# Kernel optimization log

Hardware: AMD Instinct MI355X
Metric: run time of the kernel (lower is better)

The kernel has to match this reference:

```python
import jax, jax.numpy as jnp
import numpy as np

N_X, DIS, IN, OUT = 40000, 10000, 128, 64
N = N_X + DIS
E = 800000
BN_EPS = 1e-5


def setup_inputs() -> dict:
    key = jax.random.key(0)
    ks = jax.random.split(key, 20)

    def glorot(k, shape):
        fan_in, fan_out = shape[-2], shape[-1]
        a = np.sqrt(6.0 / (fan_in + fan_out)).astype(np.float32)
        return jax.random.uniform(k, shape, jnp.float32, -a, a)

    return {
        "x": jax.random.normal(ks[0], (N_X, IN), jnp.float32),
        "emb": jax.random.uniform(ks[1], (DIS, IN), jnp.float32),
        "conv1_w": glorot(ks[2], (3, IN, 2 * OUT)),
        "conv1_root": glorot(ks[3], (IN, 2 * OUT)),
        "conv1_bias": jnp.zeros((2 * OUT,), jnp.float32),
        "conv2_w": glorot(ks[4], (3, 2 * OUT, 4 * OUT)),
        "conv2_root": glorot(ks[5], (2 * OUT, 4 * OUT)),
        "conv2_bias": jnp.zeros((4 * OUT,), jnp.float32),
        "convinf_w": glorot(ks[6], (3, 4 * OUT, 4 * OUT)),
        "convinf_root": glorot(ks[7], (4 * OUT, 4 * OUT)),
        "convinf_bias": jnp.zeros((4 * OUT,), jnp.float32),
        "conv3_w": glorot(ks[8], (3, 4 * OUT, OUT)),
        "conv3_root": glorot(ks[9], (4 * OUT, OUT)),
        "conv3_bias": jnp.zeros((OUT,), jnp.float32),
        "norm1_g": jnp.ones((2 * OUT,), jnp.float32),
        "norm1_b": jnp.zeros((2 * OUT,), jnp.float32),
        "norm2_g": jnp.ones((4 * OUT,), jnp.float32),
        "norm2_b": jnp.zeros((4 * OUT,), jnp.float32),
        "edge_index": jax.random.randint(ks[10], (2, E), 0, N),
        "edge_types": jax.random.randint(ks[11], (E,), 0, 3),
    }


def reference(x, emb, conv1_w, conv1_root, conv1_bias, conv2_w, conv2_root,
              conv2_bias, convinf_w, convinf_root, convinf_bias, conv3_w,
              conv3_root, conv3_bias, norm1_g, norm1_b, norm2_g, norm2_b,
              edge_index, edge_types):
    dst, src = edge_index[0], edge_index[1]  # adj_t row = target, col = source
    n = x.shape[0] + emb.shape[0]

    # gcn_norm without self-loops: deg over rows, w_e = d^-1/2[dst] * d^-1/2[src]
    deg = jax.ops.segment_sum(jnp.ones(dst.shape[0], jnp.float32), dst, num_segments=n)
    dis = jnp.where(deg > 0, jax.lax.rsqrt(jnp.maximum(deg, 1.0)), 0.0)
    ew = dis[dst] * dis[src]  # [E]

    def wrgcn(h, W, root, bias):
        out = h @ root + bias
        h_src = h[src]  # [E, d] gather (dominant memory traffic)
        for r in range(3):
            w_r = jnp.where(edge_types == r, ew, 0.0)
            agg = jax.ops.segment_sum(w_r[:, None] * h_src, dst, num_segments=n)
            out = out + agg @ W[r]
        return out

    def bn(h, g, b):
        m = h.mean(axis=0)
        v = jnp.var(h, axis=0)  # biased, matches torch BN training normalization
        return (h - m) * jax.lax.rsqrt(v + BN_EPS) * g + b

    h0 = jnp.concatenate([x, emb], axis=0)  # [N, IN]
    x1 = bn(wrgcn(h0, conv1_w, conv1_root, conv1_bias), norm1_g, norm1_b)
    x2 = bn(wrgcn(jax.nn.relu(x1), conv2_w, conv2_root, conv2_bias), norm2_g, norm2_b)
    for _ in range(5):
        x2 = bn(wrgcn(jax.nn.relu(x2), convinf_w, convinf_root, convinf_bias), norm2_g, norm2_b)
    return wrgcn(jax.nn.relu(x2), conv3_w, conv3_root, conv3_bias)
```

## Files before the change

kernel.cpp:

```cpp
#include <hip/hip_runtime.h>

#define N_X  40000
#define NN   50000
#define NE   800000
#define MPAD 50048

using short8  = __attribute__((ext_vector_type(8))) short;
using floatx4 = __attribute__((ext_vector_type(4))) float;

typedef const __attribute__((address_space(1))) void gv_t;
typedef __attribute__((address_space(3))) void lv_t;

__device__ __forceinline__ unsigned short f2bf(float f) {
  unsigned u = __float_as_uint(f);
  u += 0x7FFF + ((u >> 16) & 1);
  return (unsigned short)(u >> 16);
}
__device__ __forceinline__ float bf2f(unsigned v) {
  return __uint_as_float(v << 16);
}

__global__ void k_deg(const int* __restrict__ dst, int* __restrict__ deg) {
  int e = blockIdx.x * blockDim.x + threadIdx.x;
  if (e < NE) atomicAdd(&deg[dst[e]], 1);
}

__global__ void k_dis(const int* __restrict__ deg, float* __restrict__ dis) {
  int i = blockIdx.x * blockDim.x + threadIdx.x;
  if (i < NN) dis[i] = deg[i] > 0 ? rsqrtf((float)deg[i]) : 0.f;
}

#define SCAN_B 1024
#define SCAN_NB 49
__global__ void k_scan1(const int* __restrict__ deg, int* __restrict__ rowp,
                        int* __restrict__ bsum) {
  __shared__ int buf[SCAN_B];
  int b = blockIdx.x;
  int i = b * SCAN_B + threadIdx.x;
  int v = (i < NN) ? deg[i] : 0;
  buf[threadIdx.x] = v;
  __syncthreads();
  for (int off = 1; off < SCAN_B; off <<= 1) {
    int t = (threadIdx.x >= off) ? buf[threadIdx.x - off] : 0;
    __syncthreads();
    buf[threadIdx.x] += t;
    __syncthreads();
  }
  if (i < NN) rowp[i] = buf[threadIdx.x] - v;
  if (threadIdx.x == SCAN_B - 1) bsum[b] = buf[SCAN_B - 1];
}

__global__ void k_scan2(int* __restrict__ bsum) {
  if (threadIdx.x == 0) {
    int acc = 0;
    for (int i = 0; i < SCAN_NB; ++i) { int t = bsum[i]; bsum[i] = acc; acc += t; }
  }
}

__global__ void k_scan3(int* __restrict__ rowp, const int* __restrict__ bsum) {
  int i = blockIdx.x * blockDim.x + threadIdx.x;
  if (i < NN) rowp[i] += bsum[i >> 10];
  if (i == 0) rowp[NN] = NE;
}

__global__ void k_build(const int* __restrict__ dst, const int* __restrict__ src,
                        const int* __restrict__ typ, const float* __restrict__ dis,
                        const int* __restrict__ rowp, int* __restrict__ cur,
                        unsigned* __restrict__ est, float* __restrict__ ewt) {
  int e = blockIdx.x * blockDim.x + threadIdx.x;
  if (e >= NE) return;
  int d = dst[e], s = src[e];
  int p = rowp[d] + atomicAdd(&cur[d], 1);
  est[p] = (unsigned)s | ((unsigned)typ[e] << 28);
  ewt[p] = dis[d] * dis[s];
}

__global__ void k_prep0(const float* __restrict__ x, const float* __restrict__ emb,
                        unsigned short* __restrict__ Xh, unsigned short* __restrict__ Xl,
                        int xs) {
  int idx = blockIdx.x * blockDim.x + threadIdx.x;
  if (idx >= NN * 32) return;
  int r = idx >> 5, c4 = (idx & 31) * 4;
  const float* srcp = (r < N_X) ? (x + (size_t)r * 128 + c4)
                                : (emb + (size_t)(r - N_X) * 128 + c4);
  float4 hv = *(const float4*)srcp;
  float vv[4] = {hv.x, hv.y, hv.z, hv.w};
  unsigned hw[2], lw[2];
#pragma unroll
  for (int q = 0; q < 2; ++q) {
    unsigned short h0 = f2bf(vv[2 * q]), h1 = f2bf(vv[2 * q + 1]);
    unsigned short l0 = f2bf(vv[2 * q] - bf2f(h0)), l1 = f2bf(vv[2 * q + 1] - bf2f(h1));
    hw[q] = (unsigned)h0 | ((unsigned)h1 << 16);
    lw[q] = (unsigned)l0 | ((unsigned)l1 << 16);
  }
  size_t o = (size_t)r * xs + c4;
  *(uint2*)(Xh + o) = make_uint2(hw[0], hw[1]);
  *(uint2*)(Xl + o) = make_uint2(lw[0], lw[1]);
}

__global__ void k_prep(const float* __restrict__ H, const float* __restrict__ sc,
                       const float* __restrict__ sh, unsigned short* __restrict__ Xh,
                       unsigned short* __restrict__ Xl, int din, int logq, int xs) {
  int idx = blockIdx.x * blockDim.x + threadIdx.x;
  if (idx >= NN * (din >> 2)) return;
  int r = idx >> logq, c4 = (idx & ((din >> 2) - 1)) * 4;
  float4 hv = *(const float4*)(H + (size_t)r * din + c4);
  float vv[4] = {hv.x, hv.y, hv.z, hv.w};
  unsigned hw[2], lw[2];
#pragma unroll
  for (int q = 0; q < 4; ++q)
    vv[q] = fmaxf(vv[q] * sc[c4 + q] + sh[c4 + q], 0.f);
#pragma unroll
  for (int q = 0; q < 2; ++q) {
    unsigned short h0 = f2bf(vv[2 * q]), h1 = f2bf(vv[2 * q + 1]);
    unsigned short l0 = f2bf(vv[2 * q] - bf2f(h0)), l1 = f2bf(vv[2 * q + 1] - bf2f(h1));
    hw[q] = (unsigned)h0 | ((unsigned)h1 << 16);
    lw[q] = (unsigned)l0 | ((unsigned)l1 << 16);
  }
  size_t o = (size_t)r * xs + c4;
  *(uint2*)(Xh + o) = make_uint2(hw[0], hw[1]);
  *(uint2*)(Xl + o) = make_uint2(lw[0], lw[1]);
}

template <int L>
__global__ void k_agg(unsigned short* __restrict__ Xh, unsigned short* __restrict__ Xl,
                      const int* __restrict__ rowp, const unsigned* __restrict__ est,
                      const float* __restrict__ ewt, int xs) {
  constexpr int G = 64 / L;
  constexpr int din = L * 8;
  const int wid = (blockIdx.x * 256 + threadIdx.x) >> 6;
  if (wid >= NN) return;
  const int lane = threadIdx.x & 63;
  const int grp = lane / L;
  const int j = lane & (L - 1);
  const int c0 = j * 8;
  const int beg = rowp[wid], end = rowp[wid + 1];
  float a0[8] = {}, a1[8] = {}, a2[8] = {};
  for (int i = beg + grp; i < end; i += G) {
    const unsigned st = est[i];
    const float wv = ewt[i];
    const size_t off = (size_t)(st & 0x0FFFFFFFu) * xs + c0;
    const unsigned t = st >> 28;
    uint4 hr = *(const uint4*)(Xh + off);
    uint4 lr = *(const uint4*)(Xl + off);
    float v[8];
    v[0] = bf2f(hr.x & 0xFFFFu) + bf2f(lr.x & 0xFFFFu);
    v[1] = bf2f(hr.x >> 16)     + bf2f(lr.x >> 16);
    v[2] = bf2f(hr.y & 0xFFFFu) + bf2f(lr.y & 0xFFFFu);
    v[3] = bf2f(hr.y >> 16)     + bf2f(lr.y >> 16);
    v[4] = bf2f(hr.z & 0xFFFFu) + bf2f(lr.z & 0xFFFFu);
    v[5] = bf2f(hr.z >> 16)     + bf2f(lr.z >> 16);
    v[6] = bf2f(hr.w & 0xFFFFu) + bf2f(lr.w & 0xFFFFu);
    v[7] = bf2f(hr.w >> 16)     + bf2f(lr.w >> 16);
    if (t == 0) {
#pragma unroll
      for (int q = 0; q < 8; ++q) a0[q] += wv * v[q];
    } else if (t == 1) {
#pragma unroll
      for (int q = 0; q < 8; ++q) a1[q] += wv * v[q];
    } else {
#pragma unroll
      for (int q = 0; q < 8; ++q) a2[q] += wv * v[q];
    }
  }
#pragma unroll
  for (int off = L; off < 64; off <<= 1) {
#pragma unroll
    for (int q = 0; q < 8; ++q) {
      a0[q] += __shfl_xor(a0[q], off);
      a1[q] += __shfl_xor(a1[q], off);
      a2[q] += __shfl_xor(a2[q], off);
    }
  }
  if (grp == 0) {
    const size_t ob = (size_t)wid * xs + din + c0;
    auto store8 = [&](const float* a, size_t o) {
      unsigned hw[4], lw[4];
#pragma unroll
      for (int q = 0; q < 4; ++q) {
        unsigned short h0 = f2bf(a[2 * q]), h1 = f2bf(a[2 * q + 1]);
        unsigned short l0 = f2bf(a[2 * q] - bf2f(h0)), l1 = f2bf(a[2 * q + 1] - bf2f(h1));
        hw[q] = (unsigned)h0 | ((unsigned)h1 << 16);
        lw[q] = (unsigned)l0 | ((unsigned)l1 << 16);
      }
      *(uint4*)(Xh + o) = make_uint4(hw[0], hw[1], hw[2], hw[3]);
      *(uint4*)(Xl + o) = make_uint4(lw[0], lw[1], lw[2], lw[3]);
    };
    store8(a0, ob);
    store8(a1, ob + din);
    store8(a2, ob + 2 * din);
  }
}

__global__ void k_wcatT(const float* __restrict__ root, const float* __restrict__ W,
                        unsigned short* __restrict__ BhT, unsigned short* __restrict__ BlT,
                        int din, int dout) {
  int idx = blockIdx.x * blockDim.x + threadIdx.x;
  int K = 4 * din;
  if (idx >= dout * K) return;
  int n = idx / K, k = idx % K;
  float v = (k < din) ? root[(size_t)k * dout + n] : W[(size_t)(k - din) * dout + n];
  unsigned short h = f2bf(v);
  BhT[idx] = h;
  BlT[idx] = f2bf(v - bf2f(h));
}

template <int BN>
__global__ __launch_bounds__(256, (BN == 128 ? 2 : 3)) void k_gemm_mfma(
    const unsigned short* __restrict__ Ah, const unsigned short* __restrict__ Al,
    const unsigned short* __restrict__ Bh, const unsigned short* __restrict__ Bl,
    const float* __restrict__ bias, float* __restrict__ C,
    float* __restrict__ bns, int M, int K, int Nc, int ny) {
  constexpr int NCHB = BN / 16;
  constexpr int TC = 16 + 2 * NCHB;
  constexpr int CPW = TC / 4;
  constexpr int NT = BN / 32;
  __shared__ __align__(16) char lds[2][TC * 1024];

  const int tid = threadIdx.x;
  const int lane = tid & 63;
  const int w = tid >> 6;
  const int wm = w >> 1, wn = w & 1;
  const int r16 = lane & 15, kg = lane >> 4;

  const int nwg = gridDim.x;
  const int q = nwg >> 3, r = nwg & 7;
  const int xcd = blockIdx.x & 7, pos = blockIdx.x >> 3;
  const int t = (xcd < r ? xcd * (q + 1) : r * (q + 1) + (xcd - r) * q) + pos;
  const int bm = (t / ny) * 128;
  const int bn = (t % ny) * BN;

  const int rowseg = lane >> 2, seg = lane & 3;
  const unsigned short* gb[CPW];
#pragma unroll
  for (int i = 0; i < CPW; ++i) {
    int c = w * CPW + i;
    const unsigned short* base;
    int row0;
    if (c < 8)               { base = Ah; row0 = bm + c * 16; }
    else if (c < 16)         { base = Al; row0 = bm + (c - 8) * 16; }
    else if (c < 16 + NCHB)  { base = Bh; row0 = bn + (c - 16) * 16; }
    else                     { base = Bl; row0 = bn + (c - 16 - NCHB) * 16; }
    gb[i] = base + (size_t)(row0 + rowseg) * K + seg * 8;
  }

  floatx4 acc[4][NT];
#pragma unroll
  for (int i = 0; i < 4; ++i)
#pragma unroll
    for (int jj = 0; jj < NT; ++jj) acc[i][jj] = (floatx4)0.f;

  const int nk = K >> 5;

  auto stage = [&](int b, int tk) {
#pragma unroll
    for (int i = 0; i < CPW; ++i)
      __builtin_amdgcn_global_load_lds((gv_t*)(gb[i] + tk * 32),
                                       (lv_t*)&lds[b][(w * CPW + i) * 1024],
                                       16, 0, 0);
  };

  stage(0, 0);
  stage(1, 1);

  const int fo = r16 * 64 + kg * 16;

  int buf = 0;
  for (int tk = 0; tk < nk; ++tk) {
    if (tk < nk - 1) {
      if constexpr (CPW == 6)       asm volatile("s_waitcnt vmcnt(6)" ::: "memory");
      else                          asm volatile("s_waitcnt vmcnt(8)" ::: "memory");
    } else {
      asm volatile("s_waitcnt vmcnt(0)" ::: "memory");
    }
    __builtin_amdgcn_s_barrier();

    const char* Lb = lds[buf];
    short8 ah[4], al[4], bh[NT], bl[NT];
#pragma unroll
    for (int mt = 0; mt < 4; ++mt) {
      ah[mt] = *(const short8*)(Lb + (wm * 4 + mt) * 1024 + fo);
      al[mt] = *(const short8*)(Lb + (8 + wm * 4 + mt) * 1024 + fo);
    }
#pragma unroll
    for (int nt = 0; nt < NT; ++nt) {
      bh[nt] = *(const short8*)(Lb + (16 + wn * NT + nt) * 1024 + fo);
      bl[nt] = *(const short8*)(Lb + (16 + NCHB + wn * NT + nt) * 1024 + fo);
    }

    __builtin_amdgcn_s_setprio(1);
#pragma unroll
    for (int mt = 0; mt < 4; ++mt)
#pragma unroll
      for (int nt = 0; nt < NT; ++nt) {
        acc[mt][nt] = __builtin_amdgcn_mfma_f32_16x16x32_bf16(ah[mt], bh[nt], acc[mt][nt], 0, 0, 0);
        acc[mt][nt] = __builtin_amdgcn_mfma_f32_16x16x32_bf16(ah[mt], bl[nt], acc[mt][nt], 0, 0, 0);
        acc[mt][nt] = __builtin_amdgcn_mfma_f32_16x16x32_bf16(al[mt], bh[nt], acc[mt][nt], 0, 0, 0);
      }
    __builtin_amdgcn_s_setprio(0);

    __builtin_amdgcn_s_barrier();
    if (tk + 2 < nk) stage(buf, tk + 2);
    buf ^= 1;
  }

  float s[NT], s2[NT];
#pragma unroll
  for (int nt = 0; nt < NT; ++nt) { s[nt] = 0.f; s2[nt] = 0.f; }
#pragma unroll
  for (int mt = 0; mt < 4; ++mt) {
    const int gr0 = bm + wm * 64 + mt * 16 + kg * 4;
#pragma unroll
    for (int nt = 0; nt < NT; ++nt) {
      const int col = bn + wn * (NT * 16) + nt * 16 + r16;
      const float bv = bias[col];
#pragma unroll
      for (int rr = 0; rr < 4; ++rr) {
        const int gr = gr0 + rr;
        if (gr < M) {
          const float o = acc[mt][nt][rr] + bv;
          C[(size_t)gr * Nc + col] = o;
          s[nt] += o;
          s2[nt] += o * o;
        }
      }
    }
  }
  if (bns) {
#pragma unroll
    for (int nt = 0; nt < NT; ++nt) {
      float a = s[nt], b2 = s2[nt];
      a += __shfl_xor(a, 16); a += __shfl_xor(a, 32);
      b2 += __shfl_xor(b2, 16); b2 += __shfl_xor(b2, 32);
      if (kg == 0) {
        const int col = bn + wn * (NT * 16) + nt * 16 + r16;
        atomicAdd(&bns[col], a);
        atomicAdd(&bns[Nc + col], b2);
      }
    }
  }
}

__global__ void k_bnfinal(const float* __restrict__ sums, const float* __restrict__ g,
                          const float* __restrict__ b, float* __restrict__ sc,
                          float* __restrict__ sh, int d) {
  int c = threadIdx.x;
  if (c >= d) return;
  float mean = sums[c] * (1.f / NN);
  float var = sums[d + c] * (1.f / NN) - mean * mean;
  float rs = rsqrtf(var + 1e-5f);
  float s = rs * g[c];
  sc[c] = s;
  sh[c] = b[c] - mean * s;
}

extern "C" void kernel_launch(void* const* d_in, const int* in_sizes, int n_in,
                              void* d_out, int out_size, void* d_ws, size_t ws_size,
                              hipStream_t stream) {
  const float* x   = (const float*)d_in[0];
  const float* emb = (const float*)d_in[1];
  const float* conv_w[4] = {(const float*)d_in[2], (const float*)d_in[5],
                            (const float*)d_in[8], (const float*)d_in[11]};
  const float* conv_r[4] = {(const float*)d_in[3], (const float*)d_in[6],
                            (const float*)d_in[9], (const float*)d_in[12]};
  const float* conv_b[4] = {(const float*)d_in[4], (const float*)d_in[7],
                            (const float*)d_in[10], (const float*)d_in[13]};
  const float* n1g = (const float*)d_in[14];
  const float* n1b = (const float*)d_in[15];
  const float* n2g = (const float*)d_in[16];
  const float* n2b = (const float*)d_in[17];
  const int* eidx = (const int*)d_in[18];
  const int* etyp = (const int*)d_in[19];
  const int* dst  = eidx;
  const int* srcp = eidx + NE;
  float* out = (float*)d_out;

  char* w = (char*)d_ws;
  auto alloc = [&](size_t bytes) {
    char* p = w;
    w += (bytes + 255) & ~(size_t)255;
    return p;
  };
  unsigned short* Xh  = (unsigned short*)alloc((size_t)MPAD * 1024 * 2);
  unsigned short* Xl  = (unsigned short*)alloc((size_t)MPAD * 1024 * 2);
  float*    H    = (float*)alloc((size_t)NN * 256 * 4);
  unsigned short* WcTh = (unsigned short*)alloc((size_t)256 * 1024 * 2);
  unsigned short* WcTl = (unsigned short*)alloc((size_t)256 * 1024 * 2);
  float*    bns  = (float*)alloc(512 * 4);
  float*    bsc  = (float*)alloc(256 * 4);
  float*    bsh  = (float*)alloc(256 * 4);
  float*    dis  = (float*)alloc((size_t)NN * 4);
  int*      deg  = (int*)alloc((size_t)NN * 4);
  int*      rowp = (int*)alloc((size_t)(NN + 1) * 4);
  int*      cur  = (int*)alloc((size_t)NN * 4);
  int*      bsum = (int*)alloc(64 * 4);
  unsigned* est  = (unsigned*)alloc((size_t)NE * 4);
  float*    ewt  = (float*)alloc((size_t)NE * 4);

  hipMemsetAsync(deg, 0, (size_t)NN * 4, stream);
  hipMemsetAsync(cur, 0, (size_t)NN * 4, stream);
  k_deg<<<(NE + 255) / 256, 256, 0, stream>>>(dst, deg);
  k_dis<<<(NN + 255) / 256, 256, 0, stream>>>(deg, dis);
  k_scan1<<<SCAN_NB, SCAN_B, 0, stream>>>(deg, rowp, bsum);
  k_scan2<<<1, 64, 0, stream>>>(bsum);
  k_scan3<<<(NN + 255) / 256, 256, 0, stream>>>(rowp, bsum);
  k_build<<<(NE + 255) / 256, 256, 0, stream>>>(dst, srcp, etyp, dis, rowp, cur, est, ewt);

  const int din_a[8]  = {128, 128, 256, 256, 256, 256, 256, 256};
  const int dout_a[8] = {128, 256, 256, 256, 256, 256, 256, 64};
  const int wi_a[8]   = {0, 1, 2, 2, 2, 2, 2, 3};
  const int gm = (NN + 127) / 128;

  for (int l = 0; l < 8; ++l) {
    const int din = din_a[l], dout = dout_a[l];
    const int K = 4 * din, xs = K;
    const int wi = wi_a[l];

    if (l == 0)
      k_prep0<<<(NN * 32 + 255) / 256, 256, 0, stream>>>(x, emb, Xh, Xl, xs);
    else
      k_prep<<<(NN * (din >> 2) + 255) / 256, 256, 0, stream>>>(
          H, bsc, bsh, Xh, Xl, din, (din == 128 ? 5 : 6), xs);

    if (din == 128)
      k_agg<16><<<(NN + 3) / 4, 256, 0, stream>>>(Xh, Xl, rowp, est, ewt, xs);
    else
      k_agg<32><<<(NN + 3) / 4, 256, 0, stream>>>(Xh, Xl, rowp, est, ewt, xs);

    k_wcatT<<<(dout * K + 255) / 256, 256, 0, stream>>>(conv_r[wi], conv_w[wi], WcTh, WcTl, din, dout);

    if (l < 7) hipMemsetAsync(bns, 0, (size_t)2 * dout * 4, stream);

    float* C = (l == 7) ? out : H;
    float* bstat = (l == 7) ? nullptr : bns;
    if (dout == 64)
      k_gemm_mfma<64><<<gm, 256, 0, stream>>>(Xh, Xl, WcTh, WcTl, conv_b[wi], C, bstat, NN, K, dout, 1);
    else {
      const int ny = dout / 128;
      k_gemm_mfma<128><<<gm * ny, 256, 0, stream>>>(Xh, Xl, WcTh, WcTl, conv_b[wi], C, bstat, NN, K, dout, ny);
    }

    if (l < 7)
      k_bnfinal<<<1, 256, 0, stream>>>(bns, (l == 0) ? n1g : n2g,
                                       (l == 0) ? n1b : n2b, bsc, bsh, dout);
  }
}
```

Measured before the change: 1.848 ms.

## Split node features and aggregates into separate compact buffers for gather locality

Node features (hi/lo bf16 split) now go into a compact row buffer of width din instead of the wide 4*din concatenated row, so the per-edge gather in aggregation touches densely packed rows. Aggregated results go to a separate buffer using nontemporal stores. The GEMM loader picks between the two buffers based on the K tile index. Edge source/type and weight are packed into one 8-byte record so each edge needs a single load. The cost is extra pointer and branch logic in the GEMM staging loop.

```diff
diff --git a/kernel.cpp b/kernel.cpp
--- a/kernel.cpp
+++ b/kernel.cpp
@@ -7,6 +7,8 @@
 
 using short8  = __attribute__((ext_vector_type(8))) short;
 using floatx4 = __attribute__((ext_vector_type(4))) float;
+using uintx2  = __attribute__((ext_vector_type(2))) unsigned int;
+using uintx4  = __attribute__((ext_vector_type(4))) unsigned int;
 
 typedef const __attribute__((address_space(1))) void gv_t;
 typedef __attribute__((address_space(3))) void lv_t;
@@ -66,23 +68,24 @@
 __global__ void k_build(const int* __restrict__ dst, const int* __restrict__ src,
                         const int* __restrict__ typ, const float* __restrict__ dis,
                         const int* __restrict__ rowp, int* __restrict__ cur,
-                        unsigned* __restrict__ est, float* __restrict__ ewt) {
+                        uintx2* __restrict__ ed) {
   int e = blockIdx.x * blockDim.x + threadIdx.x;
   if (e >= NE) return;
   int d = dst[e], s = src[e];
   int p = rowp[d] + atomicAdd(&cur[d], 1);
-  est[p] = (unsigned)s | ((unsigned)typ[e] << 28);
-  ewt[p] = dis[d] * dis[s];
+  uintx2 v;
+  v.x = (unsigned)s | ((unsigned)typ[e] << 28);
+  v.y = __float_as_uint(dis[d] * dis[s]);
+  ed[p] = v;
 }
 
 __global__ void k_prep0(const float* __restrict__ x, const float* __restrict__ emb,
-                        unsigned short* __restrict__ Xh, unsigned short* __restrict__ Xl,
-                        int xs) {
+                        unsigned short* __restrict__ Gh, unsigned short* __restrict__ Gl) {
   int idx = blockIdx.x * blockDim.x + threadIdx.x;
   if (idx >= NN * 32) return;
-  int r = idx >> 5, c4 = (idx & 31) * 4;
-  const float* srcp = (r < N_X) ? (x + (size_t)r * 128 + c4)
-                                : (emb + (size_t)(r - N_X) * 128 + c4);
+  int r = idx >> 5;
+  const float* srcp = (r < N_X) ? (x + (size_t)idx * 4)
+                                : (emb + ((size_t)idx - (size_t)N_X * 32) * 4);
   float4 hv = *(const float4*)srcp;
   float vv[4] = {hv.x, hv.y, hv.z, hv.w};
   unsigned hw[2], lw[2];
@@ -93,23 +96,23 @@
     hw[q] = (unsigned)h0 | ((unsigned)h1 << 16);
     lw[q] = (unsigned)l0 | ((unsigned)l1 << 16);
   }
-  size_t o = (size_t)r * xs + c4;
-  *(uint2*)(Xh + o) = make_uint2(hw[0], hw[1]);
-  *(uint2*)(Xl + o) = make_uint2(lw[0], lw[1]);
+  size_t o = (size_t)idx * 4;
+  *(uintx2*)(Gh + o) = uintx2{hw[0], hw[1]};
+  *(uintx2*)(Gl + o) = uintx2{lw[0], lw[1]};
 }
 
 __global__ void k_prep(const float* __restrict__ H, const float* __restrict__ sc,
-                       const float* __restrict__ sh, unsigned short* __restrict__ Xh,
-                       unsigned short* __restrict__ Xl, int din, int logq, int xs) {
+                       const float* __restrict__ sh, unsigned short* __restrict__ Gh,
+                       unsigned short* __restrict__ Gl, int din) {
   int idx = blockIdx.x * blockDim.x + threadIdx.x;
   if (idx >= NN * (din >> 2)) return;
-  int r = idx >> logq, c4 = (idx & ((din >> 2) - 1)) * 4;
-  float4 hv = *(const float4*)(H + (size_t)r * din + c4);
+  int c4 = (idx & ((din >> 2) - 1)) * 4;
+  float4 hv = *(const float4*)(H + (size_t)idx * 4);
   float vv[4] = {hv.x, hv.y, hv.z, hv.w};
-  unsigned hw[2], lw[2];
 #pragma unroll
   for (int q = 0; q < 4; ++q)
     vv[q] = fmaxf(vv[q] * sc[c4 + q] + sh[c4 + q], 0.f);
+  unsigned hw[2], lw[2];
 #pragma unroll
   for (int q = 0; q < 2; ++q) {
     unsigned short h0 = f2bf(vv[2 * q]), h1 = f2bf(vv[2 * q + 1]);
@@ -117,15 +120,16 @@
     hw[q] = (unsigned)h0 | ((unsigned)h1 << 16);
     lw[q] = (unsigned)l0 | ((unsigned)l1 << 16);
   }
-  size_t o = (size_t)r * xs + c4;
-  *(uint2*)(Xh + o) = make_uint2(hw[0], hw[1]);
-  *(uint2*)(Xl + o) = make_uint2(lw[0], lw[1]);
+  size_t o = (size_t)idx * 4;
+  *(uintx2*)(Gh + o) = uintx2{hw[0], hw[1]};
+  *(uintx2*)(Gl + o) = uintx2{lw[0], lw[1]};
 }
 
 template <int L>
-__global__ void k_agg(unsigned short* __restrict__ Xh, unsigned short* __restrict__ Xl,
-                      const int* __restrict__ rowp, const unsigned* __restrict__ est,
-                      const float* __restrict__ ewt, int xs) {
+__global__ void k_agg(const unsigned short* __restrict__ Gh,
+                      const unsigned short* __restrict__ Gl,
+                      const int* __restrict__ rowp, const uintx2* __restrict__ ed,
+                      unsigned short* __restrict__ AGh, unsigned short* __restrict__ AGl) {
   constexpr int G = 64 / L;
   constexpr int din = L * 8;
   const int wid = (blockIdx.x * 256 + threadIdx.x) >> 6;
@@ -137,12 +141,12 @@
   const int beg = rowp[wid], end = rowp[wid + 1];
   float a0[8] = {}, a1[8] = {}, a2[8] = {};
   for (int i = beg + grp; i < end; i += G) {
-    const unsigned st = est[i];
-    const float wv = ewt[i];
-    const size_t off = (size_t)(st & 0x0FFFFFFFu) * xs + c0;
-    const unsigned t = st >> 28;
-    uint4 hr = *(const uint4*)(Xh + off);
-    uint4 lr = *(const uint4*)(Xl + off);
+    const uintx2 e = ed[i];
+    const float wv = __uint_as_float(e.y);
+    const size_t off = (size_t)(e.x & 0x0FFFFFFFu) * din + c0;
+    const unsigned t = e.x >> 28;
+    uintx4 hr = *(const uintx4*)(Gh + off);
+    uintx4 lr = *(const uintx4*)(Gl + off);
     float v[8];
     v[0] = bf2f(hr.x & 0xFFFFu) + bf2f(lr.x & 0xFFFFu);
     v[1] = bf2f(hr.x >> 16)     + bf2f(lr.x >> 16);
@@ -173,8 +177,9 @@
     }
   }
   if (grp == 0) {
-    const size_t ob = (size_t)wid * xs + din + c0;
+    const size_t ob = (size_t)wid * (3 * din) + c0;
     auto store8 = [&](const float* a, size_t o) {
+      uintx4 ph, pl;
       unsigned hw[4], lw[4];
 #pragma unroll
       for (int q = 0; q < 4; ++q) {
@@ -183,8 +188,10 @@
         hw[q] = (unsigned)h0 | ((unsigned)h1 << 16);
         lw[q] = (unsigned)l0 | ((unsigned)l1 << 16);
       }
-      *(uint4*)(Xh + o) = make_uint4(hw[0], hw[1], hw[2], hw[3]);
-      *(uint4*)(Xl + o) = make_uint4(lw[0], lw[1], lw[2], lw[3]);
+      ph.x = hw[0]; ph.y = hw[1]; ph.z = hw[2]; ph.w = hw[3];
+      pl.x = lw[0]; pl.y = lw[1]; pl.z = lw[2]; pl.w = lw[3];
+      __builtin_nontemporal_store(ph, (uintx4*)(AGh + o));
+      __builtin_nontemporal_store(pl, (uintx4*)(AGl + o));
     };
     store8(a0, ob);
     store8(a1, ob + din);
@@ -207,7 +214,8 @@
 
 template <int BN>
 __global__ __launch_bounds__(256, (BN == 128 ? 2 : 3)) void k_gemm_mfma(
-    const unsigned short* __restrict__ Ah, const unsigned short* __restrict__ Al,
+    const unsigned short* __restrict__ Gh, const unsigned short* __restrict__ Gl,
+    const unsigned short* __restrict__ AGh, const unsigned short* __restrict__ AGl,
     const unsigned short* __restrict__ Bh, const unsigned short* __restrict__ Bl,
     const float* __restrict__ bias, float* __restrict__ C,
     float* __restrict__ bns, int M, int K, int Nc, int ny) {
@@ -230,18 +238,31 @@
   const int bm = (t / ny) * 128;
   const int bn = (t % ny) * BN;
 
+  const int din = K >> 2;
+  const int nkA = K >> 7;
+
   const int rowseg = lane >> 2, seg = lane & 3;
-  const unsigned short* gb[CPW];
+  const unsigned short* p1[CPW];
+  const unsigned short* p2[CPW];
+  bool isA[CPW];
 #pragma unroll
   for (int i = 0; i < CPW; ++i) {
     int c = w * CPW + i;
-    const unsigned short* base;
-    int row0;
-    if (c < 8)               { base = Ah; row0 = bm + c * 16; }
-    else if (c < 16)         { base = Al; row0 = bm + (c - 8) * 16; }
-    else if (c < 16 + NCHB)  { base = Bh; row0 = bn + (c - 16) * 16; }
-    else                     { base = Bl; row0 = bn + (c - 16 - NCHB) * 16; }
-    gb[i] = base + (size_t)(row0 + rowseg) * K + seg * 8;
+    if (c < 16) {
+      int row0 = bm + (c & 7) * 16;
+      const unsigned short* g = (c < 8) ? Gh : Gl;
+      const unsigned short* a = (c < 8) ? AGh : AGl;
+      p1[i] = g + (size_t)(row0 + rowseg) * din + seg * 8;
+      p2[i] = a + (size_t)(row0 + rowseg) * (3 * din) + seg * 8;
+      isA[i] = true;
+    } else {
+      int cc = c - 16;
+      const unsigned short* b = (cc < NCHB) ? Bh : Bl;
+      int row0 = bn + (cc % NCHB) * 16;
+      p1[i] = b + (size_t)(row0 + rowseg) * K + seg * 8;
+      p2[i] = p1[i];
+      isA[i] = false;
+    }
   }
 
   floatx4 acc[4][NT];
@@ -254,10 +275,14 @@
 
   auto stage = [&](int b, int tk) {
 #pragma unroll
-    for (int i = 0; i < CPW; ++i)
-      __builtin_amdgcn_global_load_lds((gv_t*)(gb[i] + tk * 32),
+    for (int i = 0; i < CPW; ++i) {
+      const unsigned short* p;
+      if (isA[i]) p = (tk < nkA) ? p1[i] + tk * 32 : p2[i] + (tk - nkA) * 32;
+      else        p = p1[i] + tk * 32;
+      __builtin_amdgcn_global_load_lds((gv_t*)p,
                                        (lv_t*)&lds[b][(w * CPW + i) * 1024],
                                        16, 0, 0);
+    }
   };
 
   stage(0, 0);
@@ -381,8 +406,10 @@
     w += (bytes + 255) & ~(size_t)255;
     return p;
   };
-  unsigned short* Xh  = (unsigned short*)alloc((size_t)MPAD * 1024 * 2);
-  unsigned short* Xl  = (unsigned short*)alloc((size_t)MPAD * 1024 * 2);
+  unsigned short* Gh   = (unsigned short*)alloc((size_t)MPAD * 256 * 2);
+  unsigned short* Gl   = (unsigned short*)alloc((size_t)MPAD * 256 * 2);
+  unsigned short* AGh  = (unsigned short*)alloc((size_t)MPAD * 768 * 2);
+  unsigned short* AGl  = (unsigned short*)alloc((size_t)MPAD * 768 * 2);
   float*    H    = (float*)alloc((size_t)NN * 256 * 4);
   unsigned short* WcTh = (unsigned short*)alloc((size_t)256 * 1024 * 2);
   unsigned short* WcTl = (unsigned short*)alloc((size_t)256 * 1024 * 2);
@@ -394,8 +421,7 @@
   int*      rowp = (int*)alloc((size_t)(NN + 1) * 4);
   int*      cur  = (int*)alloc((size_t)NN * 4);
   int*      bsum = (int*)alloc(64 * 4);
-  unsigned* est  = (unsigned*)alloc((size_t)NE * 4);
-  float*    ewt  = (float*)alloc((size_t)NE * 4);
+  uintx2*   ed   = (uintx2*)alloc((size_t)NE * 8);
 
   hipMemsetAsync(deg, 0, (size_t)NN * 4, stream);
   hipMemsetAsync(cur, 0, (size_t)NN * 4, stream);
@@ -404,7 +430,7 @@
   k_scan1<<<SCAN_NB, SCAN_B, 0, stream>>>(deg, rowp, bsum);
   k_scan2<<<1, 64, 0, stream>>>(bsum);
   k_scan3<<<(NN + 255) / 256, 256, 0, stream>>>(rowp, bsum);
-  k_build<<<(NE + 255) / 256, 256, 0, stream>>>(dst, srcp, etyp, dis, rowp, cur, est, ewt);
+  k_build<<<(NE + 255) / 256, 256, 0, stream>>>(dst, srcp, etyp, dis, rowp, cur, ed);
 
   const int din_a[8]  = {128, 128, 256, 256, 256, 256, 256, 256};
   const int dout_a[8] = {128, 256, 256, 256, 256, 256, 256, 64};
@@ -413,19 +439,18 @@
 
   for (int l = 0; l < 8; ++l) {
     const int din = din_a[l], dout = dout_a[l];
-    const int K = 4 * din, xs = K;
+    const int K = 4 * din;
     const int wi = wi_a[l];
 
     if (l == 0)
-      k_prep0<<<(NN * 32 + 255) / 256, 256, 0, stream>>>(x, emb, Xh, Xl, xs);
+      k_prep0<<<(NN * 32 + 255) / 256, 256, 0, stream>>>(x, emb, Gh, Gl);
     else
-      k_prep<<<(NN * (din >> 2) + 255) / 256, 256, 0, stream>>>(
-          H, bsc, bsh, Xh, Xl, din, (din == 128 ? 5 : 6), xs);
+      k_prep<<<(NN * (din >> 2) + 255) / 256, 256, 0, stream>>>(H, bsc, bsh, Gh, Gl, din);
 
     if (din == 128)
-      k_agg<16><<<(NN + 3) / 4, 256, 0, stream>>>(Xh, Xl, rowp, est, ewt, xs);
+      k_agg<16><<<(NN + 3) / 4, 256, 0, stream>>>(Gh, Gl, rowp, ed, AGh, AGl);
     else
-      k_agg<32><<<(NN + 3) / 4, 256, 0, stream>>>(Xh, Xl, rowp, est, ewt, xs);
+      k_agg<32><<<(NN + 3) / 4, 256, 0, stream>>>(Gh, Gl, rowp, ed, AGh, AGl);
 
     k_wcatT<<<(dout * K + 255) / 256, 256, 0, stream>>>(conv_r[wi], conv_w[wi], WcTh, WcTl, din, dout);
 
@@ -434,10 +459,10 @@
     float* C = (l == 7) ? out : H;
     float* bstat = (l == 7) ? nullptr : bns;
     if (dout == 64)
-      k_gemm_mfma<64><<<gm, 256, 0, stream>>>(Xh, Xl, WcTh, WcTl, conv_b[wi], C, bstat, NN, K, dout, 1);
+      k_gemm_mfma<64><<<gm, 256, 0, stream>>>(Gh, Gl, AGh, AGl, WcTh, WcTl, conv_b[wi], C, bstat, NN, K, dout, 1);
     else {
       const int ny = dout / 128;
-      k_gemm_mfma<128><<<gm * ny, 256, 0, stream>>>(Xh, Xl, WcTh, WcTl, conv_b[wi], C, bstat, NN, K, dout, ny);
+      k_gemm_mfma<128><<<gm * ny, 256, 0, stream>>>(Gh, Gl, AGh, AGl, WcTh, WcTl, conv_b[wi], C, bstat, NN, K, dout, ny);
     }
 
     if (l < 7)
```

Measured after the change: 1.960 ms. 1.06x slower.
